# Performance work log

Hardware: AMD Instinct MI355X
Metric: run time of the kernel (lower is better)

The kernel has to match this reference:

```python
import jax, jax.numpy as jnp
import numpy as np

N, D, H = 6144, 768, 3
DH = D // H

def _lrelu(v):
    return jnp.where(v >= 0, v, 0.2 * v)

def setup_inputs() -> dict:
    key = jax.random.key(0)
    ks = jax.random.split(key, 8)
    s = 1.0 / np.sqrt(D)  # xavier-ish scale for D->D linears
    return {
        "x": jax.random.normal(ks[0], (N, D), dtype=jnp.float32),
        "adj_matrix": jax.random.randint(ks[1], (N, N), 0, 2, dtype=jnp.int32),
        "W_fc": jax.random.normal(ks[2], (D, D), dtype=jnp.float32) * s,
        "b_fc": jnp.zeros((D,), dtype=jnp.float32),
        "W_qfc": jax.random.normal(ks[3], (D, D), dtype=jnp.float32) * s,
        "b_qfc": jnp.zeros((D,), dtype=jnp.float32),
        "W_final": jax.random.normal(ks[4], (D, D), dtype=jnp.float32) * s,
        "b_final": jnp.zeros((D,), dtype=jnp.float32),
    }

def reference(x, adj_matrix, W_fc, b_fc, W_qfc, b_qfc, W_final, b_final):
    # x: [N, D], adj_matrix: [N, N] (0/1). Dropout is identity at eval.
    x_new = _lrelu(x @ W_fc.T + b_fc)          # [N, D]
    q = _lrelu(x_new @ W_qfc.T + b_qfc)        # [N, D]
    # torch.split(dim=2) into 3 contiguous chunks then cat on dim 0 == reshape heads
    xh = x_new.reshape(N, H, DH).transpose(1, 0, 2)   # [3, N, DH]
    qh = q.reshape(N, H, DH).transpose(1, 0, 2)       # [3, N, DH]
    scores = jnp.einsum('hnd,hmd->hnm', qh, xh) / 10.0  # [3, N, N]
    mask = (adj_matrix == 0)[None, :, :]                 # [1, N, N] -> broadcast
    scores = jnp.where(mask, -jnp.inf, scores)
    attn = jax.nn.softmax(scores, axis=-1)               # [3, N, N]
    out = jnp.einsum('hnm,hmd->hnd', attn, xh)           # [3, N, DH]
    out = out.transpose(1, 0, 2).reshape(N, D)           # cat heads on feature dim
    out = x + out                                        # residual 1
    ret = x + _lrelu(out @ W_final.T + b_final)          # residual 2
    return ret
```

## Files before the change

kernel.cpp:

```cpp
#include <hip/hip_runtime.h>
#include <stdint.h>

#define N_TOK 6144
#define DMODEL 768
#define NHEAD 3
#define DHEAD 256
#define NWORDS (N_TOK/32)
#define NT NWORDS

typedef __bf16 bf16x8 __attribute__((ext_vector_type(8)));
typedef float f32x4 __attribute__((ext_vector_type(4)));
typedef unsigned short u16;
typedef u16 u16x8 __attribute__((ext_vector_type(8)));
typedef u16 u16x4 __attribute__((ext_vector_type(4)));
typedef unsigned int u32;

__device__ __forceinline__ u16 f2bf(float f) {
  __bf16 b = (__bf16)f;
  return __builtin_bit_cast(u16, b);
}
__device__ __forceinline__ float bf2f(u16 u) {
  union { u32 u; float f; } v; v.u = (u32)u << 16; return v.f;
}
__device__ __forceinline__ float lrelu(float v) { return v >= 0.f ? v : 0.2f * v; }

__global__ __launch_bounds__(256) void pack_adj(const int* __restrict__ adj,
                                                u32* __restrict__ bits) {
  size_t wid = (size_t)blockIdx.x * 256 + threadIdx.x;
  const int4* p = reinterpret_cast<const int4*>(adj + wid * 32);
  u32 m = 0;
#pragma unroll
  for (int i = 0; i < 8; ++i) {
    int4 v = p[i];
    m |= (v.x != 0 ? 1u : 0u) << (i * 4 + 0);
    m |= (v.y != 0 ? 1u : 0u) << (i * 4 + 1);
    m |= (v.z != 0 ? 1u : 0u) << (i * 4 + 2);
    m |= (v.w != 0 ? 1u : 0u) << (i * 4 + 3);
  }
  bits[wid] = m;
}

__global__ __launch_bounds__(256) void transpose_bf(const u16* __restrict__ src,
                                                    u16* __restrict__ dst) {
  __shared__ u16 t[64][72];
  const int n0 = blockIdx.x * 64, d0 = blockIdx.y * 64;
  const int tid = threadIdx.x;
#pragma unroll
  for (int i = 0; i < 2; ++i) {
    int c = tid + i * 256;
    int r = c >> 3, c8 = (c & 7) * 8;
    *reinterpret_cast<u16x8*>(&t[r][c8]) =
        *reinterpret_cast<const u16x8*>(src + (size_t)(n0 + r) * DMODEL + d0 + c8);
  }
  __syncthreads();
#pragma unroll
  for (int i = 0; i < 2; ++i) {
    int c = tid + i * 256;
    int dr = c >> 3, n8 = (c & 7) * 8;
    u16x8 v;
#pragma unroll
    for (int j = 0; j < 8; ++j) v[j] = t[n8 + j][dr];
    *reinterpret_cast<u16x8*>(dst + (size_t)(d0 + dr) * N_TOK + n0 + n8) = v;
  }
}

__global__ void init_knmax(u32* knmax2) {
  if (threadIdx.x < NHEAD) knmax2[threadIdx.x] = 0;
}

__global__ __launch_bounds__(256) void knorm_max(const u16* __restrict__ xnew,
                                                 u32* __restrict__ knmax2) {
  int n = blockIdx.x * 256 + threadIdx.x;
  int h = blockIdx.y;
  const u16* row = xnew + (size_t)n * DMODEL + h * DHEAD;
  float s = 0.f;
#pragma unroll 4
  for (int i = 0; i < 32; ++i) {
    u16x8 v = *reinterpret_cast<const u16x8*>(row + i * 8);
#pragma unroll
    for (int j = 0; j < 8; ++j) { float f = bf2f(v[j]); s += f * f; }
  }
#pragma unroll
  for (int off = 1; off < 64; off <<= 1) s = fmaxf(s, __shfl_xor(s, off));
  if ((threadIdx.x & 63) == 0) atomicMax(knmax2 + h, __float_as_uint(s));
}

__global__ __launch_bounds__(256) void qbound(const u16* __restrict__ qbf,
                                              const u32* __restrict__ knmax2,
                                              float* __restrict__ Mrow) {
  int n = blockIdx.x * 256 + threadIdx.x;
  int h = blockIdx.y;
  const u16* row = qbf + (size_t)n * DMODEL + h * DHEAD;
  float s = 0.f;
#pragma unroll 4
  for (int i = 0; i < 32; ++i) {
    u16x8 v = *reinterpret_cast<const u16x8*>(row + i * 8);
#pragma unroll
    for (int j = 0; j < 8; ++j) { float f = bf2f(v[j]); s += f * f; }
  }
  float kn2 = __uint_as_float(knmax2[h]);
  Mrow[(size_t)h * N_TOK + n] = sqrtf(s * kn2);
}

template <int ABF, int FINAL>
__global__ __launch_bounds__(256) void gemm_nt(const void* __restrict__ Aptr,
                                               const float* __restrict__ W,
                                               const float* __restrict__ bias,
                                               const float* __restrict__ resid,
                                               u16* __restrict__ out_bf,
                                               float* __restrict__ out_f,
                                               float oscale) {
  __shared__ u16 As[128][72];
  __shared__ u16 Bs[128][72];
  const int tid = threadIdx.x;
  const int w = tid >> 6, lane = tid & 63, lr = lane & 15, lg = lane >> 4;
  const int m0 = blockIdx.x * 128, n0 = blockIdx.y * 128;
  const int wr = (w >> 1) * 64, wc = (w & 1) * 64;
  f32x4 acc[4][4] = {};
  for (int kt = 0; kt < DMODEL / 64; ++kt) {
    __syncthreads();
#pragma unroll
    for (int i = 0; i < 4; ++i) {
      int c = tid + i * 256;
      int row = c >> 3, c8 = (c & 7) * 8;
      int gcol = kt * 64 + c8;
      if (ABF) {
        *reinterpret_cast<u16x8*>(&As[row][c8]) = *reinterpret_cast<const u16x8*>(
            (const u16*)Aptr + (size_t)(m0 + row) * DMODEL + gcol);
      } else {
        const float* src = (const float*)Aptr + (size_t)(m0 + row) * DMODEL + gcol;
        float4 f0 = *reinterpret_cast<const float4*>(src);
        float4 f1 = *reinterpret_cast<const float4*>(src + 4);
        u16x8 v = {f2bf(f0.x), f2bf(f0.y), f2bf(f0.z), f2bf(f0.w),
                   f2bf(f1.x), f2bf(f1.y), f2bf(f1.z), f2bf(f1.w)};
        *reinterpret_cast<u16x8*>(&As[row][c8]) = v;
      }
      const float* wsrc = W + (size_t)(n0 + row) * DMODEL + gcol;
      float4 g0 = *reinterpret_cast<const float4*>(wsrc);
      float4 g1 = *reinterpret_cast<const float4*>(wsrc + 4);
      u16x8 wv = {f2bf(g0.x), f2bf(g0.y), f2bf(g0.z), f2bf(g0.w),
                  f2bf(g1.x), f2bf(g1.y), f2bf(g1.z), f2bf(g1.w)};
      *reinterpret_cast<u16x8*>(&Bs[row][c8]) = wv;
    }
    __syncthreads();
#pragma unroll
    for (int ks = 0; ks < 2; ++ks) {
      bf16x8 a[4], b[4];
#pragma unroll
      for (int mi = 0; mi < 4; ++mi)
        a[mi] = *reinterpret_cast<const bf16x8*>(&As[wr + mi * 16 + lr][ks * 32 + lg * 8]);
#pragma unroll
      for (int ni = 0; ni < 4; ++ni)
        b[ni] = *reinterpret_cast<const bf16x8*>(&Bs[wc + ni * 16 + lr][ks * 32 + lg * 8]);
#pragma unroll
      for (int mi = 0; mi < 4; ++mi)
#pragma unroll
        for (int ni = 0; ni < 4; ++ni)
          acc[mi][ni] =
              __builtin_amdgcn_mfma_f32_16x16x32_bf16(a[mi], b[ni], acc[mi][ni], 0, 0, 0);
    }
  }
#pragma unroll
  for (int mi = 0; mi < 4; ++mi)
#pragma unroll
    for (int ni = 0; ni < 4; ++ni)
#pragma unroll
      for (int r = 0; r < 4; ++r) {
        int grow = m0 + wr + mi * 16 + lg * 4 + r;
        int gcol = n0 + wc + ni * 16 + lr;
        float v = lrelu(acc[mi][ni][r] + bias[gcol]);
        size_t idx = (size_t)grow * DMODEL + gcol;
        if (FINAL)
          out_f[idx] = resid[idx] + v;
        else
          out_bf[idx] = f2bf(v * oscale);
      }
}

template <int SPLIT>
__global__ __launch_bounds__(256) void attn_fused(
    const u16* __restrict__ Kmat,
    const u16* __restrict__ Qmat,
    const u16* __restrict__ VT,
    const u32* __restrict__ bits,
    const float* __restrict__ Mrow,
    const float* __restrict__ x,
    u16* __restrict__ out2,
    float* __restrict__ Opart,
    float* __restrict__ lpart) {
  __shared__ u16 Ks[32][264];
  __shared__ u16 Vs[256][36];
  __shared__ u16 Ps[4][16][40];
  const int tid = threadIdx.x;
  const int w = tid >> 6, lane = tid & 63, lr = lane & 15, lg = lane >> 4;
  const int q0 = blockIdx.x * 64;
  const int h = blockIdx.y;
  const int z = blockIdx.z;
  const int qrow = q0 + w * 16 + lr;

  bf16x8 qf[8];
  {
    const u16* qrowp = Qmat + (size_t)qrow * DMODEL + h * DHEAD + lg * 8;
#pragma unroll
    for (int s = 0; s < 8; ++s) qf[s] = *reinterpret_cast<const bf16x8*>(qrowp + s * 32);
  }
  const float Mr = Mrow[(size_t)h * N_TOK + qrow];
  f32x4 o[16] = {};
  float lsum = 0.f;

  const int t0 = z * (NT / SPLIT), t1 = t0 + NT / SPLIT;

  u16x8 kst[4], vst[4];
  u32 wnext, wcur;

  auto issue_tile = [&](int kt) {
#pragma unroll
    for (int i = 0; i < 4; ++i) {
      int c = tid + i * 256;
      int kr = c >> 5, kc = (c & 31) * 8;
      kst[i] = *reinterpret_cast<const u16x8*>(
          Kmat + (size_t)(kt * 32 + kr) * DMODEL + h * DHEAD + kc);
      int vr = c >> 2, vc = (c & 3) * 8;
      vst[i] = *reinterpret_cast<const u16x8*>(
          VT + (size_t)(h * DHEAD + vr) * N_TOK + kt * 32 + vc);
    }
    wnext = bits[(size_t)qrow * NWORDS + kt];
  };
  auto write_tile = [&]() {
#pragma unroll
    for (int i = 0; i < 4; ++i) {
      int c = tid + i * 256;
      int kr = c >> 5, kc = (c & 31) * 8;
      *reinterpret_cast<u16x8*>(&Ks[kr][kc]) = kst[i];
      int vr = c >> 2, vc = (c & 3) * 8;
      *reinterpret_cast<u16x8*>(&Vs[vr][vc]) = vst[i];
    }
  };

  issue_tile(t0);

  for (int kt = t0; kt < t1; ++kt) {
    __syncthreads();
    write_tile();
    wcur = wnext;
    if (kt + 1 < t1) issue_tile(kt + 1);
    __syncthreads();

    f32x4 st[2] = {};
#pragma unroll
    for (int s = 0; s < 8; ++s) {
      bf16x8 k0 = *reinterpret_cast<const bf16x8*>(&Ks[lr][s * 32 + lg * 8]);
      bf16x8 k1 = *reinterpret_cast<const bf16x8*>(&Ks[16 + lr][s * 32 + lg * 8]);
      st[0] = __builtin_amdgcn_mfma_f32_16x16x32_bf16(k0, qf[s], st[0], 0, 0, 0);
      st[1] = __builtin_amdgcn_mfma_f32_16x16x32_bf16(k1, qf[s], st[1], 0, 0, 0);
    }
#pragma unroll
    for (int kb = 0; kb < 2; ++kb) {
      u16x4 pk;
#pragma unroll
      for (int r = 0; r < 4; ++r) {
        int keyl = kb * 16 + lg * 4 + r;
        float pe = ((wcur >> keyl) & 1u) ? __expf(st[kb][r] - Mr) : 0.f;
        lsum += pe;
        pk[r] = f2bf(pe);
      }
      *reinterpret_cast<u16x4*>(&Ps[w][lr][kb * 16 + lg * 4]) = pk;
    }
    asm volatile("s_waitcnt lgkmcnt(0)" ::: "memory");
    __builtin_amdgcn_sched_barrier(0);
    bf16x8 pf = *reinterpret_cast<const bf16x8*>(&Ps[w][lr][lg * 8]);
#pragma unroll
    for (int d = 0; d < 16; ++d) {
      bf16x8 vf = *reinterpret_cast<const bf16x8*>(&Vs[d * 16 + lr][lg * 8]);
      o[d] = __builtin_amdgcn_mfma_f32_16x16x32_bf16(pf, vf, o[d], 0, 0, 0);
    }
  }

  lsum += __shfl_xor(lsum, 16);
  lsum += __shfl_xor(lsum, 32);

  if (SPLIT == 1) {
    float ls[4];
#pragma unroll
    for (int r = 0; r < 4; ++r) ls[r] = __shfl(lsum, lg * 4 + r);
#pragma unroll
    for (int d = 0; d < 16; ++d)
#pragma unroll
      for (int r = 0; r < 4; ++r) {
        int grow = q0 + w * 16 + lg * 4 + r;
        int gcol = h * DHEAD + d * 16 + lr;
        size_t idx = (size_t)grow * DMODEL + gcol;
        out2[idx] = f2bf(x[idx] + o[d][r] / ls[r]);
      }
  } else {
    float* Op = Opart + (size_t)z * N_TOK * DMODEL;
#pragma unroll
    for (int d = 0; d < 16; ++d)
#pragma unroll
      for (int r = 0; r < 4; ++r) {
        int grow = q0 + w * 16 + lg * 4 + r;
        int gcol = h * DHEAD + d * 16 + lr;
        Op[(size_t)grow * DMODEL + gcol] = o[d][r];
      }
    if (lane < 16)
      lpart[((size_t)z * NHEAD + h) * N_TOK + qrow] = lsum;
  }
}

template <int SPLIT>
__global__ __launch_bounds__(256) void attn_combine(const float* __restrict__ Opart,
                                                    const float* __restrict__ lpart,
                                                    const float* __restrict__ x,
                                                    u16* __restrict__ out2) {
  int g = blockIdx.x * 256 + threadIdx.x;
  int q = g / (DMODEL / 4);
  int col = (g % (DMODEL / 4)) * 4;
  int h = col >> 8;
  float L = 0.f;
#pragma unroll
  for (int s = 0; s < SPLIT; ++s)
    L += lpart[((size_t)s * NHEAD + h) * N_TOK + q];
  float rL = 1.f / L;
  size_t idx = (size_t)q * DMODEL + col;
  float4 acc = make_float4(0.f, 0.f, 0.f, 0.f);
#pragma unroll
  for (int s = 0; s < SPLIT; ++s) {
    float4 O = *reinterpret_cast<const float4*>(Opart + (size_t)s * N_TOK * DMODEL + idx);
    acc.x += O.x; acc.y += O.y; acc.z += O.z; acc.w += O.w;
  }
  float4 xv = *reinterpret_cast<const float4*>(x + idx);
  u16x4 r;
  r[0] = f2bf(xv.x + acc.x * rL);
  r[1] = f2bf(xv.y + acc.y * rL);
  r[2] = f2bf(xv.z + acc.z * rL);
  r[3] = f2bf(xv.w + acc.w * rL);
  *reinterpret_cast<u16x4*>(out2 + idx) = r;
}

extern "C" void kernel_launch(void* const* d_in, const int* in_sizes, int n_in,
                              void* d_out, int out_size, void* d_ws, size_t ws_size,
                              hipStream_t stream) {
  const float* x     = (const float*)d_in[0];
  const int*   adj   = (const int*)d_in[1];
  const float* W_fc  = (const float*)d_in[2];
  const float* b_fc  = (const float*)d_in[3];
  const float* W_qfc = (const float*)d_in[4];
  const float* b_qfc = (const float*)d_in[5];
  const float* W_fin = (const float*)d_in[6];
  const float* b_fin = (const float*)d_in[7];
  float* out = (float*)d_out;

  char* ws = (char*)d_ws;
  size_t off = 0;
  auto alloc = [&](size_t bytes) {
    char* p = ws + off;
    off += (bytes + 255) & ~(size_t)255;
    return p;
  };
  u16* xnew_bf = (u16*)alloc((size_t)N_TOK * DMODEL * 2);
  u16* q_bf    = (u16*)alloc((size_t)N_TOK * DMODEL * 2);
  u16* xT      = (u16*)alloc((size_t)DMODEL * N_TOK * 2);
  u16* out2_bf = (u16*)alloc((size_t)N_TOK * DMODEL * 2);
  u32* bits    = (u32*)alloc((size_t)N_TOK * NWORDS * 4);
  u32* knmax2  = (u32*)alloc(NHEAD * 4);
  float* Mrow  = (float*)alloc((size_t)NHEAD * N_TOK * 4);
  size_t base_off = off;
  float* Opart = (float*)alloc((size_t)6 * N_TOK * DMODEL * 4);
  float* lpart = (float*)alloc((size_t)6 * NHEAD * N_TOK * 4);
  size_t need6 = off;
  auto needN = [&](size_t n) {
    return base_off + (((size_t)n * N_TOK * DMODEL * 4 + 255) & ~(size_t)255) +
           (((size_t)n * NHEAD * N_TOK * 4 + 255) & ~(size_t)255);
  };
  const int split = (ws_size >= need6) ? 6
                  : (ws_size >= needN(4)) ? 4
                  : (ws_size >= needN(2)) ? 2 : 1;

  pack_adj<<<N_TOK * NWORDS / 256, 256, 0, stream>>>(adj, bits);
  dim3 ggrid(N_TOK / 128, DMODEL / 128);
  gemm_nt<0, 0><<<ggrid, 256, 0, stream>>>(x, W_fc, b_fc, nullptr, xnew_bf, nullptr, 1.0f);
  gemm_nt<1, 0><<<ggrid, 256, 0, stream>>>(xnew_bf, W_qfc, b_qfc, nullptr, q_bf, nullptr,
                                           0.1f);
  transpose_bf<<<dim3(N_TOK / 64, DMODEL / 64), 256, 0, stream>>>(xnew_bf, xT);
  init_knmax<<<1, 64, 0, stream>>>(knmax2);
  dim3 bgrid(N_TOK / 256, NHEAD);
  knorm_max<<<bgrid, 256, 0, stream>>>(xnew_bf, knmax2);
  qbound<<<bgrid, 256, 0, stream>>>(q_bf, knmax2, Mrow);
  dim3 cgrid(N_TOK * DMODEL / 4 / 256);
  if (split == 6) {
    attn_fused<6><<<dim3(N_TOK / 64, NHEAD, 6), 256, 0, stream>>>(
        xnew_bf, q_bf, xT, bits, Mrow, x, out2_bf, Opart, lpart);
    attn_combine<6><<<cgrid, 256, 0, stream>>>(Opart, lpart, x, out2_bf);
  } else if (split == 4) {
    attn_fused<4><<<dim3(N_TOK / 64, NHEAD, 4), 256, 0, stream>>>(
        xnew_bf, q_bf, xT, bits, Mrow, x, out2_bf, Opart, lpart);
    attn_combine<4><<<cgrid, 256, 0, stream>>>(Opart, lpart, x, out2_bf);
  } else if (split == 2) {
    attn_fused<2><<<dim3(N_TOK / 64, NHEAD, 2), 256, 0, stream>>>(
        xnew_bf, q_bf, xT, bits, Mrow, x, out2_bf, Opart, lpart);
    attn_combine<2><<<cgrid, 256, 0, stream>>>(Opart, lpart, x, out2_bf);
  } else {
    attn_fused<1><<<dim3(N_TOK / 64, NHEAD, 1), 256, 0, stream>>>(
        xnew_bf, q_bf, xT, bits, Mrow, x, out2_bf, Opart, lpart);
  }
  gemm_nt<1, 1><<<ggrid, 256, 0, stream>>>(out2_bf, W_fin, b_fin, x, nullptr, out, 1.0f);
}
```

Measured before the change: 363.3 us.

## Halve GEMM M-tile and share P across warps in attention PV product

The projection GEMMs switch from 128x128 to 64x128 tiles, doubling the grid so more workgroups fill the GPU's compute units. In the attention kernel, each warp now multiplies two query groups' P tiles against half of the V columns. Each V fragment is read once from LDS and reused for two MFMAs, where before every warp read all 16 V fragments. This needs a block-wide __syncthreads per key tile in place of a per-warp wait. The SPLIT==1 epilogue now passes row sums through shared memory.

```diff
diff --git a/kernel.cpp b/kernel.cpp
--- a/kernel.cpp
+++ b/kernel.cpp
@@ -110,17 +110,17 @@
                                                u16* __restrict__ out_bf,
                                                float* __restrict__ out_f,
                                                float oscale) {
-  __shared__ u16 As[128][72];
+  __shared__ u16 As[64][72];
   __shared__ u16 Bs[128][72];
   const int tid = threadIdx.x;
   const int w = tid >> 6, lane = tid & 63, lr = lane & 15, lg = lane >> 4;
-  const int m0 = blockIdx.x * 128, n0 = blockIdx.y * 128;
-  const int wr = (w >> 1) * 64, wc = (w & 1) * 64;
-  f32x4 acc[4][4] = {};
+  const int m0 = blockIdx.x * 64, n0 = blockIdx.y * 128;
+  const int wr = (w >> 1) * 32, wc = (w & 1) * 64;
+  f32x4 acc[2][4] = {};
   for (int kt = 0; kt < DMODEL / 64; ++kt) {
     __syncthreads();
 #pragma unroll
-    for (int i = 0; i < 4; ++i) {
+    for (int i = 0; i < 2; ++i) {
       int c = tid + i * 256;
       int row = c >> 3, c8 = (c & 7) * 8;
       int gcol = kt * 64 + c8;
@@ -135,6 +135,12 @@
                    f2bf(f1.x), f2bf(f1.y), f2bf(f1.z), f2bf(f1.w)};
         *reinterpret_cast<u16x8*>(&As[row][c8]) = v;
       }
+    }
+#pragma unroll
+    for (int i = 0; i < 4; ++i) {
+      int c = tid + i * 256;
+      int row = c >> 3, c8 = (c & 7) * 8;
+      int gcol = kt * 64 + c8;
       const float* wsrc = W + (size_t)(n0 + row) * DMODEL + gcol;
       float4 g0 = *reinterpret_cast<const float4*>(wsrc);
       float4 g1 = *reinterpret_cast<const float4*>(wsrc + 4);
@@ -145,15 +151,15 @@
     __syncthreads();
 #pragma unroll
     for (int ks = 0; ks < 2; ++ks) {
-      bf16x8 a[4], b[4];
-#pragma unroll
-      for (int mi = 0; mi < 4; ++mi)
+      bf16x8 a[2], b[4];
+#pragma unroll
+      for (int mi = 0; mi < 2; ++mi)
         a[mi] = *reinterpret_cast<const bf16x8*>(&As[wr + mi * 16 + lr][ks * 32 + lg * 8]);
 #pragma unroll
       for (int ni = 0; ni < 4; ++ni)
         b[ni] = *reinterpret_cast<const bf16x8*>(&Bs[wc + ni * 16 + lr][ks * 32 + lg * 8]);
 #pragma unroll
-      for (int mi = 0; mi < 4; ++mi)
+      for (int mi = 0; mi < 2; ++mi)
 #pragma unroll
         for (int ni = 0; ni < 4; ++ni)
           acc[mi][ni] =
@@ -161,7 +167,7 @@
     }
   }
 #pragma unroll
-  for (int mi = 0; mi < 4; ++mi)
+  for (int mi = 0; mi < 2; ++mi)
 #pragma unroll
     for (int ni = 0; ni < 4; ++ni)
 #pragma unroll
@@ -191,12 +197,15 @@
   __shared__ u16 Ks[32][264];
   __shared__ u16 Vs[256][36];
   __shared__ u16 Ps[4][16][40];
+  __shared__ float lss[64];
   const int tid = threadIdx.x;
   const int w = tid >> 6, lane = tid & 63, lr = lane & 15, lg = lane >> 4;
   const int q0 = blockIdx.x * 64;
   const int h = blockIdx.y;
   const int z = blockIdx.z;
   const int qrow = q0 + w * 16 + lr;
+  const int qp = (w >> 1) * 2;
+  const int dbase = (w & 1) * 8;
 
   bf16x8 qf[8];
   {
@@ -205,7 +214,7 @@
     for (int s = 0; s < 8; ++s) qf[s] = *reinterpret_cast<const bf16x8*>(qrowp + s * 32);
   }
   const float Mr = Mrow[(size_t)h * N_TOK + qrow];
-  f32x4 o[16] = {};
+  f32x4 o[2][8] = {};
   float lsum = 0.f;
 
   const int t0 = z * (NT / SPLIT), t1 = t0 + NT / SPLIT;
@@ -266,13 +275,15 @@
       }
       *reinterpret_cast<u16x4*>(&Ps[w][lr][kb * 16 + lg * 4]) = pk;
     }
-    asm volatile("s_waitcnt lgkmcnt(0)" ::: "memory");
-    __builtin_amdgcn_sched_barrier(0);
-    bf16x8 pf = *reinterpret_cast<const bf16x8*>(&Ps[w][lr][lg * 8]);
-#pragma unroll
-    for (int d = 0; d < 16; ++d) {
-      bf16x8 vf = *reinterpret_cast<const bf16x8*>(&Vs[d * 16 + lr][lg * 8]);
-      o[d] = __builtin_amdgcn_mfma_f32_16x16x32_bf16(pf, vf, o[d], 0, 0, 0);
+    __syncthreads();
+
+    bf16x8 pf0 = *reinterpret_cast<const bf16x8*>(&Ps[qp][lr][lg * 8]);
+    bf16x8 pf1 = *reinterpret_cast<const bf16x8*>(&Ps[qp + 1][lr][lg * 8]);
+#pragma unroll
+    for (int d = 0; d < 8; ++d) {
+      bf16x8 vf = *reinterpret_cast<const bf16x8*>(&Vs[(dbase + d) * 16 + lr][lg * 8]);
+      o[0][d] = __builtin_amdgcn_mfma_f32_16x16x32_bf16(pf0, vf, o[0][d], 0, 0, 0);
+      o[1][d] = __builtin_amdgcn_mfma_f32_16x16x32_bf16(pf1, vf, o[1][d], 0, 0, 0);
     }
   }
 
@@ -280,28 +291,32 @@
   lsum += __shfl_xor(lsum, 32);
 
   if (SPLIT == 1) {
-    float ls[4];
-#pragma unroll
-    for (int r = 0; r < 4; ++r) ls[r] = __shfl(lsum, lg * 4 + r);
-#pragma unroll
-    for (int d = 0; d < 16; ++d)
-#pragma unroll
-      for (int r = 0; r < 4; ++r) {
-        int grow = q0 + w * 16 + lg * 4 + r;
-        int gcol = h * DHEAD + d * 16 + lr;
-        size_t idx = (size_t)grow * DMODEL + gcol;
-        out2[idx] = f2bf(x[idx] + o[d][r] / ls[r]);
-      }
+    if (lane < 16) lss[w * 16 + lr] = lsum;
+    __syncthreads();
+#pragma unroll
+    for (int t = 0; t < 2; ++t)
+#pragma unroll
+      for (int d = 0; d < 8; ++d)
+#pragma unroll
+        for (int r = 0; r < 4; ++r) {
+          int grow = q0 + (w >> 1) * 32 + t * 16 + lg * 4 + r;
+          int gcol = h * DHEAD + (w & 1) * 128 + d * 16 + lr;
+          size_t idx = (size_t)grow * DMODEL + gcol;
+          float ls = lss[(w >> 1) * 32 + t * 16 + lg * 4 + r];
+          out2[idx] = f2bf(x[idx] + o[t][d][r] / ls);
+        }
   } else {
     float* Op = Opart + (size_t)z * N_TOK * DMODEL;
 #pragma unroll
-    for (int d = 0; d < 16; ++d)
-#pragma unroll
-      for (int r = 0; r < 4; ++r) {
-        int grow = q0 + w * 16 + lg * 4 + r;
-        int gcol = h * DHEAD + d * 16 + lr;
-        Op[(size_t)grow * DMODEL + gcol] = o[d][r];
-      }
+    for (int t = 0; t < 2; ++t)
+#pragma unroll
+      for (int d = 0; d < 8; ++d)
+#pragma unroll
+        for (int r = 0; r < 4; ++r) {
+          int grow = q0 + (w >> 1) * 32 + t * 16 + lg * 4 + r;
+          int gcol = h * DHEAD + (w & 1) * 128 + d * 16 + lr;
+          Op[(size_t)grow * DMODEL + gcol] = o[t][d][r];
+        }
     if (lane < 16)
       lpart[((size_t)z * NHEAD + h) * N_TOK + qrow] = lsum;
   }
@@ -377,7 +392,7 @@
                   : (ws_size >= needN(2)) ? 2 : 1;
 
   pack_adj<<<N_TOK * NWORDS / 256, 256, 0, stream>>>(adj, bits);
-  dim3 ggrid(N_TOK / 128, DMODEL / 128);
+  dim3 ggrid(N_TOK / 64, DMODEL / 128);
   gemm_nt<0, 0><<<ggrid, 256, 0, stream>>>(x, W_fc, b_fc, nullptr, xnew_bf, nullptr, 1.0f);
   gemm_nt<1, 0><<<ggrid, 256, 0, stream>>>(xnew_bf, W_qfc, b_qfc, nullptr, q_bf, nullptr,
                                            0.1f);
```

Measured after the change: 385.8 us. 6.2% more time.
